# Kernel tuning notes

Measured on AMD Instinct MI355X. Metric: run time of the kernel, lower is better.

Reference implementation:

```python
import jax, jax.numpy as jnp
import numpy as np

UNITS = 64

def _tri_indices(u):
    # pairs (a,b) with b>=a in row-major order == tf.boolean_mask(product_mask1)
    pairs = [(a, b) for a in range(u) for b in range(a, u)]
    ia = np.array([p[0] for p in pairs], np.int32)
    ib = np.array([p[1] for p in pairs], np.int32)
    # triples: for product1 index p=(a,b), keep c>=b (derived from mask2 loops)
    ip, ic = [], []
    for p, (a, b) in enumerate(pairs):
        for c in range(b, u):
            ip.append(p)
            ic.append(c)
    return ia, ib, np.array(ip, np.int32), np.array(ic, np.int32)

def setup_inputs() -> dict:
    key = jax.random.key(0)
    k0, k1, k2, k3, k4 = jax.random.split(key, 5)
    B, D, u = 4096, 66, UNITS
    nprod1 = u * (u + 1) // 2            # 2080
    nprod2 = u * (u + 1) * (u + 2) // 6  # 45760
    inputs = jax.random.normal(k0, (B, D), jnp.float32)
    fw1 = jax.random.uniform(k1, (u,), jnp.float32, 0.0, 2.0 * np.pi * 40.0)
    fw2 = jax.random.normal(k2, (u,), jnp.float32) * 0.05
    fb1 = jax.random.normal(k3, (u,), jnp.float32) * 0.05
    wo = jax.random.normal(k4, (u + nprod1 + nprod2, u), jnp.float32) * 0.05
    return {"inputs": inputs, "fw1": fw1, "fw2": fw2, "fb1": fb1, "wo": wo}

def reference(inputs, fw1, fw2, fb1, wo):
    u = fw1.shape[0]
    ia, ib, ip, ic = _tri_indices(u)
    # Fourier features: cos(x * w1 + b1) * w2,  [B, u]
    f = jnp.cos(inputs[:, :u] * fw1 + fb1) * fw2
    # quadratic upper-triangular products, [B, nprod1] (gather instead of dense outer+mask)
    p1 = f[:, ia] * f[:, ib]
    # cubic products c>=b>=a, [B, nprod2]
    p2 = p1[:, ip] * f[:, ic]
    comb = jnp.concatenate([f, p1, p2], axis=1)  # [B, u+nprod1+nprod2]
    pad = jnp.zeros((inputs.shape[0], inputs.shape[1] - u), inputs.dtype)
    return jnp.concatenate([comb @ wo, pad], axis=1) + inputs
```

## Files before the change

kernel.cpp:

```cpp
#include <hip/hip_runtime.h>
#include <hip/hip_bf16.h>

#define NB      4096
#define ND      66
#define NSTEP   1748
#define KS      48
#define CH      37
#define MB      16
#define FS      72

#define WBLK    (NSTEP*8)
#define FBLK    (NB*FS/256)
#define PBLK    32

typedef __attribute__((ext_vector_type(8))) _Float16 f16x8;
typedef __attribute__((ext_vector_type(4))) _Float16 f16x4;
typedef __attribute__((ext_vector_type(4))) float    f32x4;

__device__ __attribute__((aligned(16))) _Float16 g_f[NB * FS];
__device__ __attribute__((aligned(16))) _Float16 g_woTi[(size_t)(NSTEP + 1) * 2048];
__device__ __attribute__((aligned(16))) _Float16 g_part[(size_t)KS * MB * 4 * 16 * 256];

__constant__ int c_bb[8] = {0, 48, 204, 532, 1096, 1960, 3188, 4844};

__device__ inline unsigned octet_desc(int o) {
    int t = 0;
#pragma unroll
    for (int i = 1; i < 8; ++i) t += (o >= c_bb[i]);
    int li = o - c_bb[t];
    int P = 8 * t + 8, T = P * (P + 1) / 2;
    int s0, s1;
    if (li == 0)       { s0 = 64; s1 = 64; }
    else if (li <= P)  { s0 = li - 1; s1 = 64; }
    else if (li <= P + T) {
        int r = li - P - 1, a = 0;
        while (r >= P - a) { r -= P - a; ++a; }
        s0 = a; s1 = a + r;
    } else             { s0 = 65; s1 = 65; }
    return (unsigned)s0 | ((unsigned)s1 << 8) | ((unsigned)(8 * t) << 16);
}

__global__ void k_prep(const float* __restrict__ inp, const float* __restrict__ fw1,
                       const float* __restrict__ fw2, const float* __restrict__ fb1,
                       const float* __restrict__ wo, float* __restrict__ out) {
    const int bid = blockIdx.x, tid = threadIdx.x;
    if (bid < WBLK) {
        int e = bid * 256 + tid;
        int s = e >> 11, r = e & 2047;
        int q = r >> 9, gg = (r >> 7) & 3, rl = (r >> 3) & 15, j = r & 7;
        unsigned d = octet_desc(s * 4 + gg);
        int s0 = d & 255, s1 = (d >> 8) & 255, cb = d >> 16;
        int n = q * 16 + rl;
        float val = 0.0f;
        if (s0 < 64) {
            if (s1 == 64) {
                int a = s0, b = cb + j;
                if (b >= a) val = wo[(64 + a * (129 - a) / 2 + (b - a)) * 64 + n];
            } else {
                int a = s0, b = s1, c = cb + j;
                if (c >= b) {
                    int TP = 45760 - (64 - a) * (65 - a) * (66 - a) / 6;
                    int RB = b * (129 - b) / 2 - a * (129 - a) / 2;
                    val = wo[(2144 + TP + RB + (c - b)) * 64 + n];
                }
            }
        } else if (s0 == 64) {
            val = wo[(cb + j) * 64 + n];
        }
        g_woTi[e] = (_Float16)val;
    } else if (bid < WBLK + FBLK) {
        int i = (bid - WBLK) * 256 + tid;
        int r = i / FS, c = i - r * FS;
        float v;
        if (c < 64)       v = cosf(inp[r * ND + c] * fw1[c] + fb1[c]) * fw2[c];
        else if (c == 64) v = 1.0f;
        else              v = 0.0f;
        g_f[i] = (_Float16)v;
    } else {
        int i = (bid - WBLK - FBLK) * 256 + tid;
        int r = i >> 1, c = 64 + (i & 1);
        out[r * ND + c] = inp[r * ND + c];
    }
}

__global__ __launch_bounds__(256, 3) void k_gemm() {
    __shared__ __attribute__((aligned(16))) _Float16 fl[256 * FS];
    __shared__ unsigned ldesc[CH * 4];
    const int mb = blockIdx.x, ks = blockIdx.y, tid = threadIdx.x;
    const int s0c = ks * CH;
    const int s1c = (s0c + CH < NSTEP) ? s0c + CH : NSTEP;
    const int ns = s1c - s0c;

    {
        const uint4* src = (const uint4*)(g_f + (size_t)mb * 256 * FS);
        uint4* dst = (uint4*)fl;
        for (int e = tid; e < 256 * FS * 2 / 16; e += 256) dst[e] = src[e];
        for (int e = tid; e < ns * 4; e += 256) ldesc[e] = octet_desc(s0c * 4 + e);
    }
    __syncthreads();

    const int wave = tid >> 6, lane = tid & 63, rl = lane & 15, g = lane >> 4;
    const _Float16* fr0 = fl + (wave * 64 +  0 + rl) * FS;
    const _Float16* fr1 = fl + (wave * 64 + 16 + rl) * FS;
    const _Float16* fr2 = fl + (wave * 64 + 32 + rl) * FS;
    const _Float16* fr3 = fl + (wave * 64 + 48 + rl) * FS;

    f32x4 acc[4][4];
#pragma unroll
    for (int a = 0; a < 4; ++a)
#pragma unroll
        for (int q = 0; q < 4; ++q) acc[a][q] = f32x4{0.f, 0.f, 0.f, 0.f};

    f16x8 c0{}, c1{}, c2{}, c3{};
    _Float16 fa0 = 0, fa1 = 0, fa2 = 0, fa3 = 0;
    int cbPrev = -1;
    unsigned dPrev = 0xFFFFFFFFu;

    const _Float16* bptr = g_woTi + (size_t)s0c * 2048 + lane * 8;
    f16x8 B0 = *(const f16x8*)(bptr +    0);
    f16x8 B1 = *(const f16x8*)(bptr +  512);
    f16x8 B2 = *(const f16x8*)(bptr + 1024);
    f16x8 B3 = *(const f16x8*)(bptr + 1536);
    bptr += 2048;

    for (int s = s0c; s < s1c; ++s) {
        const unsigned d = ldesc[(s - s0c) * 4 + g];
        const int si0 = d & 255, si1 = (d >> 8) & 255;
        const int cb = __builtin_amdgcn_readfirstlane(d >> 16);
        if (__any((d & 255) != (dPrev & 255))) {
            fa0 = fr0[si0]; fa1 = fr1[si0]; fa2 = fr2[si0]; fa3 = fr3[si0];
        }
        dPrev = d;
        if (cb != cbPrev) {
            cbPrev = cb;
            c0 = *(const f16x8*)(fr0 + cb);
            c1 = *(const f16x8*)(fr1 + cb);
            c2 = *(const f16x8*)(fr2 + cb);
            c3 = *(const f16x8*)(fr3 + cb);
        }
        f16x8 nB0 = *(const f16x8*)(bptr +    0);
        f16x8 nB1 = *(const f16x8*)(bptr +  512);
        f16x8 nB2 = *(const f16x8*)(bptr + 1024);
        f16x8 nB3 = *(const f16x8*)(bptr + 1536);
        bptr += 2048;

        const _Float16 p0 = fa0 * fr0[si1];
        const _Float16 p1 = fa1 * fr1[si1];
        const _Float16 p2 = fa2 * fr2[si1];
        const _Float16 p3 = fa3 * fr3[si1];
        const f16x8 a0 = c0 * p0, a1 = c1 * p1, a2 = c2 * p2, a3 = c3 * p3;

        acc[0][0] = __builtin_amdgcn_mfma_f32_16x16x32_f16(a0, B0, acc[0][0], 0, 0, 0);
        acc[0][1] = __builtin_amdgcn_mfma_f32_16x16x32_f16(a0, B1, acc[0][1], 0, 0, 0);
        acc[0][2] = __builtin_amdgcn_mfma_f32_16x16x32_f16(a0, B2, acc[0][2], 0, 0, 0);
        acc[0][3] = __builtin_amdgcn_mfma_f32_16x16x32_f16(a0, B3, acc[0][3], 0, 0, 0);
        acc[1][0] = __builtin_amdgcn_mfma_f32_16x16x32_f16(a1, B0, acc[1][0], 0, 0, 0);
        acc[1][1] = __builtin_amdgcn_mfma_f32_16x16x32_f16(a1, B1, acc[1][1], 0, 0, 0);
        acc[1][2] = __builtin_amdgcn_mfma_f32_16x16x32_f16(a1, B2, acc[1][2], 0, 0, 0);
        acc[1][3] = __builtin_amdgcn_mfma_f32_16x16x32_f16(a1, B3, acc[1][3], 0, 0, 0);
        acc[2][0] = __builtin_amdgcn_mfma_f32_16x16x32_f16(a2, B0, acc[2][0], 0, 0, 0);
        acc[2][1] = __builtin_amdgcn_mfma_f32_16x16x32_f16(a2, B1, acc[2][1], 0, 0, 0);
        acc[2][2] = __builtin_amdgcn_mfma_f32_16x16x32_f16(a2, B2, acc[2][2], 0, 0, 0);
        acc[2][3] = __builtin_amdgcn_mfma_f32_16x16x32_f16(a2, B3, acc[2][3], 0, 0, 0);
        acc[3][0] = __builtin_amdgcn_mfma_f32_16x16x32_f16(a3, B0, acc[3][0], 0, 0, 0);
        acc[3][1] = __builtin_amdgcn_mfma_f32_16x16x32_f16(a3, B1, acc[3][1], 0, 0, 0);
        acc[3][2] = __builtin_amdgcn_mfma_f32_16x16x32_f16(a3, B2, acc[3][2], 0, 0, 0);
        acc[3][3] = __builtin_amdgcn_mfma_f32_16x16x32_f16(a3, B3, acc[3][3], 0, 0, 0);

        B0 = nB0; B1 = nB1; B2 = nB2; B3 = nB3;
    }

    _Float16* pp = g_part + ((((size_t)ks * MB + mb) * 4 + wave) * 16) * 256;
#pragma unroll
    for (int a = 0; a < 4; ++a)
#pragma unroll
        for (int q = 0; q < 4; ++q) {
            f16x4 v;
            v[0] = (_Float16)acc[a][q][0]; v[1] = (_Float16)acc[a][q][1];
            v[2] = (_Float16)acc[a][q][2]; v[3] = (_Float16)acc[a][q][3];
            *(f16x4*)(pp + (a * 4 + q) * 256 + lane * 4) = v;
        }
}

__global__ void k_reduce(const float* __restrict__ inp, float* __restrict__ out) {
    int t = blockIdx.x * 256 + threadIdx.x;
    int c = t & 63, rg = t >> 6;
    int mb = rg >> 6, wave = (rg >> 4) & 3, a = (rg >> 2) & 3, g = rg & 3;
    int q = c >> 4, rl = c & 15, lane = g * 16 + rl;
    int rbase = mb * 256 + wave * 64 + a * 16 + g * 4;
    float acc[4];
#pragma unroll
    for (int i2 = 0; i2 < 4; ++i2) acc[i2] = inp[(rbase + i2) * ND + c];
    const _Float16* pp = g_part + ((((size_t)mb * 4 + wave) * 16) + a * 4 + q) * 256 + lane * 4;
#pragma unroll
    for (int ks = 0; ks < KS; ++ks) {
        const f16x4 p = *(const f16x4*)(pp + (size_t)ks * MB * 4 * 16 * 256);
#pragma unroll
        for (int i2 = 0; i2 < 4; ++i2) acc[i2] += (float)p[i2];
    }
#pragma unroll
    for (int i2 = 0; i2 < 4; ++i2) out[(rbase + i2) * ND + c] = acc[i2];
}

extern "C" void kernel_launch(void* const* d_in, const int* in_sizes, int n_in,
                              void* d_out, int out_size, void* d_ws, size_t ws_size,
                              hipStream_t stream) {
    const float* inp = (const float*)d_in[0];
    const float* fw1 = (const float*)d_in[1];
    const float* fw2 = (const float*)d_in[2];
    const float* fb1 = (const float*)d_in[3];
    const float* wo  = (const float*)d_in[4];
    float* out = (float*)d_out;

    k_prep<<<WBLK + FBLK + PBLK, 256, 0, stream>>>(inp, fw1, fw2, fb1, wo, out);
    k_gemm<<<dim3(MB, KS), 256, 0, stream>>>();
    k_reduce<<<256, 256, 0, stream>>>(inp, out);
}
```

Baseline: 58.95 us.

## Replace split-K partial buffer and reduce kernel with float atomics into output

```diff
diff --git a/kernel.cpp b/kernel.cpp
--- a/kernel.cpp
+++ b/kernel.cpp
@@ -3,23 +3,21 @@
 
 #define NB      4096
 #define ND      66
-#define NSTEP   1748
+#define NSTEPP  1776
 #define KS      48
 #define CH      37
 #define MB      16
 #define FS      72
 
-#define WBLK    (NSTEP*8)
+#define SBLK    NSTEPP
 #define FBLK    (NB*FS/256)
-#define PBLK    32
+#define OBLK    (NB*ND/256)
 
 typedef __attribute__((ext_vector_type(8))) _Float16 f16x8;
-typedef __attribute__((ext_vector_type(4))) _Float16 f16x4;
 typedef __attribute__((ext_vector_type(4))) float    f32x4;
 
 __device__ __attribute__((aligned(16))) _Float16 g_f[NB * FS];
-__device__ __attribute__((aligned(16))) _Float16 g_woTi[(size_t)(NSTEP + 1) * 2048];
-__device__ __attribute__((aligned(16))) _Float16 g_part[(size_t)KS * MB * 4 * 16 * 256];
+__device__ __attribute__((aligned(16))) _Float16 g_woTi[(size_t)(NSTEPP + 1) * 2048];
 
 __constant__ int c_bb[8] = {0, 48, 204, 532, 1096, 1960, 3188, 4844};
 
@@ -44,32 +42,38 @@
                        const float* __restrict__ fw2, const float* __restrict__ fb1,
                        const float* __restrict__ wo, float* __restrict__ out) {
     const int bid = blockIdx.x, tid = threadIdx.x;
-    if (bid < WBLK) {
-        int e = bid * 256 + tid;
-        int s = e >> 11, r = e & 2047;
-        int q = r >> 9, gg = (r >> 7) & 3, rl = (r >> 3) & 15, j = r & 7;
-        unsigned d = octet_desc(s * 4 + gg);
-        int s0 = d & 255, s1 = (d >> 8) & 255, cb = d >> 16;
-        int n = q * 16 + rl;
-        float val = 0.0f;
-        if (s0 < 64) {
-            if (s1 == 64) {
-                int a = s0, b = cb + j;
-                if (b >= a) val = wo[(64 + a * (129 - a) / 2 + (b - a)) * 64 + n];
-            } else {
-                int a = s0, b = s1, c = cb + j;
-                if (c >= b) {
-                    int TP = 45760 - (64 - a) * (65 - a) * (66 - a) / 6;
-                    int RB = b * (129 - b) / 2 - a * (129 - a) / 2;
-                    val = wo[(2144 + TP + RB + (c - b)) * 64 + n];
-                }
-            }
-        } else if (s0 == 64) {
-            val = wo[(cb + j) * 64 + n];
+    if (bid < SBLK) {
+        __shared__ unsigned sd[4];
+        if (tid < 4) sd[tid] = octet_desc(bid * 4 + tid);
+        __syncthreads();
+        const int q = tid >> 6, gg = (tid >> 4) & 3, rl = tid & 15;
+        const unsigned d = sd[gg];
+        const int s0 = d & 255, s1 = (d >> 8) & 255, cb = d >> 16;
+        const int n = q * 16 + rl;
+        f16x8 v;
+        if (s0 == 64) {
+#pragma unroll
+            for (int j = 0; j < 8; ++j) v[j] = (_Float16)wo[(cb + j) * 64 + n];
+        } else if (s0 < 64 && s1 == 64) {
+            int base = 64 + s0 * (129 - s0) / 2 + (cb - s0);
+#pragma unroll
+            for (int j = 0; j < 8; ++j)
+                v[j] = (cb + j >= s0) ? (_Float16)wo[(base + j) * 64 + n] : (_Float16)0.f;
+        } else if (s0 < 64) {
+            int a = s0, b = s1;
+            int TP = 45760 - (64 - a) * (65 - a) * (66 - a) / 6;
+            int RB = b * (129 - b) / 2 - a * (129 - a) / 2;
+            int base = 2144 + TP + RB + (cb - b);
+#pragma unroll
+            for (int j = 0; j < 8; ++j)
+                v[j] = (cb + j >= b) ? (_Float16)wo[(base + j) * 64 + n] : (_Float16)0.f;
+        } else {
+#pragma unroll
+            for (int j = 0; j < 8; ++j) v[j] = (_Float16)0.f;
         }
-        g_woTi[e] = (_Float16)val;
-    } else if (bid < WBLK + FBLK) {
-        int i = (bid - WBLK) * 256 + tid;
+        *(f16x8*)(g_woTi + (size_t)bid * 2048 + tid * 8) = v;
+    } else if (bid < SBLK + FBLK) {
+        int i = (bid - SBLK) * 256 + tid;
         int r = i / FS, c = i - r * FS;
         float v;
         if (c < 64)       v = cosf(inp[r * ND + c] * fw1[c] + fb1[c]) * fw2[c];
@@ -77,25 +81,25 @@
         else              v = 0.0f;
         g_f[i] = (_Float16)v;
     } else {
-        int i = (bid - WBLK - FBLK) * 256 + tid;
-        int r = i >> 1, c = 64 + (i & 1);
-        out[r * ND + c] = inp[r * ND + c];
-    }
-}
-
-__global__ __launch_bounds__(256, 3) void k_gemm() {
+        int i = (bid - SBLK - FBLK) * 256 + tid;
+        out[i] = inp[i];
+    }
+}
+
+__global__ __launch_bounds__(256, 3) void k_gemm(float* __restrict__ out) {
     __shared__ __attribute__((aligned(16))) _Float16 fl[256 * FS];
-    __shared__ unsigned ldesc[CH * 4];
+    __shared__ __attribute__((aligned(16))) unsigned ldescT[4 * 40];
     const int mb = blockIdx.x, ks = blockIdx.y, tid = threadIdx.x;
     const int s0c = ks * CH;
-    const int s1c = (s0c + CH < NSTEP) ? s0c + CH : NSTEP;
-    const int ns = s1c - s0c;
 
     {
         const uint4* src = (const uint4*)(g_f + (size_t)mb * 256 * FS);
         uint4* dst = (uint4*)fl;
         for (int e = tid; e < 256 * FS * 2 / 16; e += 256) dst[e] = src[e];
-        for (int e = tid; e < ns * 4; e += 256) ldesc[e] = octet_desc(s0c * 4 + e);
+        for (int e = tid; e < 160; e += 256) {
+            int gg = e / 40, s = e - gg * 40;
+            ldescT[e] = (s < CH) ? octet_desc((s0c + s) * 4 + gg) : (65u | (65u << 8));
+        }
     }
     __syncthreads();
 
@@ -113,8 +117,7 @@
 
     f16x8 c0{}, c1{}, c2{}, c3{};
     _Float16 fa0 = 0, fa1 = 0, fa2 = 0, fa3 = 0;
-    int cbPrev = -1;
-    unsigned dPrev = 0xFFFFFFFFu;
+    int cbPrev = -1, siPrev = -1;
 
     const _Float16* bptr = g_woTi + (size_t)s0c * 2048 + lane * 8;
     f16x8 B0 = *(const f16x8*)(bptr +    0);
@@ -123,83 +126,64 @@
     f16x8 B3 = *(const f16x8*)(bptr + 1536);
     bptr += 2048;
 
-    for (int s = s0c; s < s1c; ++s) {
-        const unsigned d = ldesc[(s - s0c) * 4 + g];
-        const int si0 = d & 255, si1 = (d >> 8) & 255;
-        const int cb = __builtin_amdgcn_readfirstlane(d >> 16);
-        if (__any((d & 255) != (dPrev & 255))) {
-            fa0 = fr0[si0]; fa1 = fr1[si0]; fa2 = fr2[si0]; fa3 = fr3[si0];
-        }
-        dPrev = d;
-        if (cb != cbPrev) {
-            cbPrev = cb;
-            c0 = *(const f16x8*)(fr0 + cb);
-            c1 = *(const f16x8*)(fr1 + cb);
-            c2 = *(const f16x8*)(fr2 + cb);
-            c3 = *(const f16x8*)(fr3 + cb);
-        }
-        f16x8 nB0 = *(const f16x8*)(bptr +    0);
-        f16x8 nB1 = *(const f16x8*)(bptr +  512);
-        f16x8 nB2 = *(const f16x8*)(bptr + 1024);
-        f16x8 nB3 = *(const f16x8*)(bptr + 1536);
-        bptr += 2048;
-
-        const _Float16 p0 = fa0 * fr0[si1];
-        const _Float16 p1 = fa1 * fr1[si1];
-        const _Float16 p2 = fa2 * fr2[si1];
-        const _Float16 p3 = fa3 * fr3[si1];
-        const f16x8 a0 = c0 * p0, a1 = c1 * p1, a2 = c2 * p2, a3 = c3 * p3;
-
-        acc[0][0] = __builtin_amdgcn_mfma_f32_16x16x32_f16(a0, B0, acc[0][0], 0, 0, 0);
-        acc[0][1] = __builtin_amdgcn_mfma_f32_16x16x32_f16(a0, B1, acc[0][1], 0, 0, 0);
-        acc[0][2] = __builtin_amdgcn_mfma_f32_16x16x32_f16(a0, B2, acc[0][2], 0, 0, 0);
-        acc[0][3] = __builtin_amdgcn_mfma_f32_16x16x32_f16(a0, B3, acc[0][3], 0, 0, 0);
-        acc[1][0] = __builtin_amdgcn_mfma_f32_16x16x32_f16(a1, B0, acc[1][0], 0, 0, 0);
-        acc[1][1] = __builtin_amdgcn_mfma_f32_16x16x32_f16(a1, B1, acc[1][1], 0, 0, 0);
-        acc[1][2] = __builtin_amdgcn_mfma_f32_16x16x32_f16(a1, B2, acc[1][2], 0, 0, 0);
-        acc[1][3] = __builtin_amdgcn_mfma_f32_16x16x32_f16(a1, B3, acc[1][3], 0, 0, 0);
-        acc[2][0] = __builtin_amdgcn_mfma_f32_16x16x32_f16(a2, B0, acc[2][0], 0, 0, 0);
-        acc[2][1] = __builtin_amdgcn_mfma_f32_16x16x32_f16(a2, B1, acc[2][1], 0, 0, 0);
-        acc[2][2] = __builtin_amdgcn_mfma_f32_16x16x32_f16(a2, B2, acc[2][2], 0, 0, 0);
-        acc[2][3] = __builtin_amdgcn_mfma_f32_16x16x32_f16(a2, B3, acc[2][3], 0, 0, 0);
-        acc[3][0] = __builtin_amdgcn_mfma_f32_16x16x32_f16(a3, B0, acc[3][0], 0, 0, 0);
-        acc[3][1] = __builtin_amdgcn_mfma_f32_16x16x32_f16(a3, B1, acc[3][1], 0, 0, 0);
-        acc[3][2] = __builtin_amdgcn_mfma_f32_16x16x32_f16(a3, B2, acc[3][2], 0, 0, 0);
-        acc[3][3] = __builtin_amdgcn_mfma_f32_16x16x32_f16(a3, B3, acc[3][3], 0, 0, 0);
-
-        B0 = nB0; B1 = nB1; B2 = nB2; B3 = nB3;
-    }
-
-    _Float16* pp = g_part + ((((size_t)ks * MB + mb) * 4 + wave) * 16) * 256;
-#pragma unroll
-    for (int a = 0; a < 4; ++a)
-#pragma unroll
-        for (int q = 0; q < 4; ++q) {
-            f16x4 v;
-            v[0] = (_Float16)acc[a][q][0]; v[1] = (_Float16)acc[a][q][1];
-            v[2] = (_Float16)acc[a][q][2]; v[3] = (_Float16)acc[a][q][3];
-            *(f16x4*)(pp + (a * 4 + q) * 256 + lane * 4) = v;
-        }
-}
-
-__global__ void k_reduce(const float* __restrict__ inp, float* __restrict__ out) {
-    int t = blockIdx.x * 256 + threadIdx.x;
-    int c = t & 63, rg = t >> 6;
-    int mb = rg >> 6, wave = (rg >> 4) & 3, a = (rg >> 2) & 3, g = rg & 3;
-    int q = c >> 4, rl = c & 15, lane = g * 16 + rl;
-    int rbase = mb * 256 + wave * 64 + a * 16 + g * 4;
-    float acc[4];
-#pragma unroll
-    for (int i2 = 0; i2 < 4; ++i2) acc[i2] = inp[(rbase + i2) * ND + c];
-    const _Float16* pp = g_part + ((((size_t)mb * 4 + wave) * 16) + a * 4 + q) * 256 + lane * 4;
-#pragma unroll
-    for (int ks = 0; ks < KS; ++ks) {
-        const f16x4 p = *(const f16x4*)(pp + (size_t)ks * MB * 4 * 16 * 256);
-#pragma unroll
-        for (int i2 = 0; i2 < 4; ++i2) acc[i2] += (float)p[i2];
-    }
-#pragma unroll
-    for (int i2 = 0; i2 < 4; ++i2) out[(rbase + i2) * ND + c] = acc[i2];
+#define STEP(dv)                                                               \
+    {                                                                          \
+        const int si0 = (dv) & 255, si1 = ((dv) >> 8) & 255;                   \
+        const int cb = __builtin_amdgcn_readfirstlane((dv) >> 16);             \
+        if (__any(si0 != siPrev)) {                                            \
+            siPrev = si0;                                                      \
+            fa0 = fr0[si0]; fa1 = fr1[si0]; fa2 = fr2[si0]; fa3 = fr3[si0];    \
+        }                                                                      \
+        if (cb != cbPrev) {                                                    \
+            cbPrev = cb;                                                       \
+            c0 = *(const f16x8*)(fr0 + cb); c1 = *(const f16x8*)(fr1 + cb);    \
+            c2 = *(const f16x8*)(fr2 + cb); c3 = *(const f16x8*)(fr3 + cb);    \
+        }                                                                      \
+        f16x8 nB0 = *(const f16x8*)(bptr +    0);                              \
+        f16x8 nB1 = *(const f16x8*)(bptr +  512);                              \
+        f16x8 nB2 = *(const f16x8*)(bptr + 1024);                              \
+        f16x8 nB3 = *(const f16x8*)(bptr + 1536);                              \
+        bptr += 2048;                                                          \
+        const _Float16 p0 = fa0 * fr0[si1], p1 = fa1 * fr1[si1];               \
+        const _Float16 p2 = fa2 * fr2[si1], p3 = fa3 * fr3[si1];               \
+        const f16x8 a0 = c0 * p0, a1 = c1 * p1, a2 = c2 * p2, a3 = c3 * p3;    \
+        acc[0][0] = __builtin_amdgcn_mfma_f32_16x16x32_f16(a0, B0, acc[0][0], 0, 0, 0); \
+        acc[0][1] = __builtin_amdgcn_mfma_f32_16x16x32_f16(a0, B1, acc[0][1], 0, 0, 0); \
+        acc[0][2] = __builtin_amdgcn_mfma_f32_16x16x32_f16(a0, B2, acc[0][2], 0, 0, 0); \
+        acc[0][3] = __builtin_amdgcn_mfma_f32_16x16x32_f16(a0, B3, acc[0][3], 0, 0, 0); \
+        acc[1][0] = __builtin_amdgcn_mfma_f32_16x16x32_f16(a1, B0, acc[1][0], 0, 0, 0); \
+        acc[1][1] = __builtin_amdgcn_mfma_f32_16x16x32_f16(a1, B1, acc[1][1], 0, 0, 0); \
+        acc[1][2] = __builtin_amdgcn_mfma_f32_16x16x32_f16(a1, B2, acc[1][2], 0, 0, 0); \
+        acc[1][3] = __builtin_amdgcn_mfma_f32_16x16x32_f16(a1, B3, acc[1][3], 0, 0, 0); \
+        acc[2][0] = __builtin_amdgcn_mfma_f32_16x16x32_f16(a2, B0, acc[2][0], 0, 0, 0); \
+        acc[2][1] = __builtin_amdgcn_mfma_f32_16x16x32_f16(a2, B1, acc[2][1], 0, 0, 0); \
+        acc[2][2] = __builtin_amdgcn_mfma_f32_16x16x32_f16(a2, B2, acc[2][2], 0, 0, 0); \
+        acc[2][3] = __builtin_amdgcn_mfma_f32_16x16x32_f16(a2, B3, acc[2][3], 0, 0, 0); \
+        acc[3][0] = __builtin_amdgcn_mfma_f32_16x16x32_f16(a3, B0, acc[3][0], 0, 0, 0); \
+        acc[3][1] = __builtin_amdgcn_mfma_f32_16x16x32_f16(a3, B1, acc[3][1], 0, 0, 0); \
+        acc[3][2] = __builtin_amdgcn_mfma_f32_16x16x32_f16(a3, B2, acc[3][2], 0, 0, 0); \
+        acc[3][3] = __builtin_amdgcn_mfma_f32_16x16x32_f16(a3, B3, acc[3][3], 0, 0, 0); \
+        B0 = nB0; B1 = nB1; B2 = nB2; B3 = nB3;                                \
+    }
+
+    const unsigned* dT = ldescT + g * 40;
+    for (int s2 = 0; s2 < 36; s2 += 2) {
+        uint2 dd = *(const uint2*)(dT + s2);
+        STEP(dd.x);
+        STEP(dd.y);
+    }
+    STEP(dT[36]);
+#undef STEP
+
+    const int rbase = mb * 256 + wave * 64 + g * 4;
+#pragma unroll
+    for (int aa = 0; aa < 4; ++aa)
+#pragma unroll
+        for (int q = 0; q < 4; ++q)
+#pragma unroll
+            for (int i2 = 0; i2 < 4; ++i2)
+                atomicAdd(&out[(size_t)(rbase + aa * 16 + i2) * ND + q * 16 + rl],
+                          acc[aa][q][i2]);
 }
 
 extern "C" void kernel_launch(void* const* d_in, const int* in_sizes, int n_in,
@@ -212,7 +196,6 @@
     const float* wo  = (const float*)d_in[4];
     float* out = (float*)d_out;
 
-    k_prep<<<WBLK + FBLK + PBLK, 256, 0, stream>>>(inp, fw1, fw2, fb1, wo, out);
-    k_gemm<<<dim3(MB, KS), 256, 0, stream>>>();
-    k_reduce<<<256, 256, 0, stream>>>(inp, out);
-}
+    k_prep<<<SBLK + FBLK + OBLK, 256, 0, stream>>>(inp, fw1, fw2, fb1, wo, out);
+    k_gemm<<<dim3(MB, KS), 256, 0, stream>>>(out);
+}
```

After: 112.1 us. +90.2%, slower.
